# Kernel optimization log

Hardware: AMD Instinct MI355X
Metric: run time of the kernel (lower is better)

Reference implementation:

```python
import jax, jax.numpy as jnp
import numpy as np

NEG_BIG = -9e15
ALPHA = 0.2  # leakyrelu negative slope


def setup_inputs() -> dict:
    key = jax.random.key(0)
    k1, k2, k3, k4 = jax.random.split(key, 4)
    N, F_in, F_out = 8192, 256, 256
    h = jax.random.normal(k1, (N, F_in), dtype=jnp.float32)
    adj = jax.random.randint(k2, (N, N), 0, 2).astype(jnp.float32)
    W = jax.random.normal(k3, (F_in, F_out), dtype=jnp.float32) * (1.414 / np.sqrt(F_in))
    a = jax.random.normal(k4, (2 * F_out, 1), dtype=jnp.float32) * (1.414 / np.sqrt(2 * F_out))
    return {"h": h, "adj": adj, "W": W, "a": a}


def reference(h, adj, W, a):
    F_out = W.shape[1]
    Wh = h @ W  # [N, F_out]
    # Decomposed additive score: e_ij = leakyrelu(a1.Wh_i + a2.Wh_j)
    # identical to matmul(cat([Wh_i, Wh_j]), a) in the original.
    a1 = a[:F_out, 0]  # [F_out]
    a2 = a[F_out:, 0]  # [F_out]
    s1 = Wh @ a1  # [N]
    s2 = Wh @ a2  # [N]
    e = jax.nn.leaky_relu(s1[:, None] + s2[None, :], negative_slope=ALPHA)  # [N, N]
    e = jnp.where(adj > 0, e, NEG_BIG)
    attention = jax.nn.softmax(e, axis=1)
    # dropout skipped (eval mode: training=False)
    h_prime = attention @ Wh  # [N, F_out]
    return jax.nn.elu(h_prime)
```

## Files before the change

kernel.cpp:

```cpp
#include <hip/hip_runtime.h>
#include <hip/hip_bf16.h>

#define N 8192
#define F 256
#define KSPLIT 4
#define JBLK (N / KSPLIT)
#define NITER (JBLK / 64)
#define LOG2E 1.4426950408889634f

using s16x8 = __attribute__((ext_vector_type(8))) short;
using f32x4 = __attribute__((ext_vector_type(4))) float;

static __device__ __forceinline__ unsigned short f2bf(float f) {
  unsigned int u = __float_as_uint(f);
  unsigned int r = u + 0x7fffu + ((u >> 16) & 1u);
  return (unsigned short)(r >> 16);
}
static __device__ __forceinline__ float bf2f(unsigned short u) {
  return __uint_as_float(((unsigned int)u) << 16);
}
static __device__ __forceinline__ void glds16(const void* g, void* l) {
  __builtin_amdgcn_global_load_lds(
      (const __attribute__((address_space(1))) unsigned int*)g,
      (__attribute__((address_space(3))) unsigned int*)l, 16, 0, 0);
}

__global__ __launch_bounds__(256) void k0_wt(const float* __restrict__ W,
                                             unsigned short* __restrict__ Wt) {
  int k = blockIdx.x;
  int f = threadIdx.x;
  Wt[f * 256 + k] = f2bf(W[k * 256 + f]);
}

__global__ __launch_bounds__(256) void k1_wh(const float* __restrict__ h,
                                             const unsigned short* __restrict__ Wt,
                                             const float* __restrict__ a,
                                             char* __restrict__ WhbT,
                                             float* __restrict__ s1g,
                                             float* __restrict__ s2g) {
  __shared__ char lds[8192 + 32768];
  char* Alds = lds;
  char* Blds = lds + 8192;
  int t = threadIdx.x;
  int i0 = blockIdx.x * 64;
  int l = t & 63, w = t >> 6;
  int lr = l & 15, lk = l >> 4;
  f32x4 acc[4][4] = {};
  for (int kt = 0; kt < 4; ++kt) {
    int k0 = kt * 64;
    if (kt) __syncthreads();
#pragma unroll
    for (int c = 0; c < 4; ++c) {
      int flat = c * 256 + t;
      int i = flat >> 4, jc = flat & 15;
      float4 v = *reinterpret_cast<const float4*>(h + (size_t)(i0 + i) * 256 + k0 + jc * 4);
      ushort4 pk;
      pk.x = f2bf(v.x); pk.y = f2bf(v.y); pk.z = f2bf(v.z); pk.w = f2bf(v.w);
      *reinterpret_cast<ushort4*>(Alds + i * 128 + ((jc * 8) ^ ((i & 7) << 4))) = pk;
    }
#pragma unroll
    for (int c = 0; c < 8; ++c) {
      int idx = c * 256 + t;
      int fr = idx >> 3, kc = idx & 7;
      uint4 v = *reinterpret_cast<const uint4*>(Wt + fr * 256 + k0 + kc * 8);
      *reinterpret_cast<uint4*>(Blds + fr * 128 + ((kc * 16) ^ ((fr & 7) << 4))) = v;
    }
    __syncthreads();
#pragma unroll
    for (int kk = 0; kk < 2; ++kk) {
      int kofs = kk * 64 + lk * 16;
      s16x8 afr[4], bfr[4];
#pragma unroll
      for (int mf = 0; mf < 4; ++mf) {
        int ar = mf * 16 + lr;
        afr[mf] = *reinterpret_cast<const s16x8*>(Alds + ar * 128 + (kofs ^ ((ar & 7) << 4)));
      }
#pragma unroll
      for (int nf = 0; nf < 4; ++nf) {
        int br = w * 64 + nf * 16 + lr;
        bfr[nf] = *reinterpret_cast<const s16x8*>(Blds + br * 128 + (kofs ^ ((br & 7) << 4)));
      }
#pragma unroll
      for (int mf = 0; mf < 4; ++mf)
#pragma unroll
        for (int nf = 0; nf < 4; ++nf)
          acc[mf][nf] = __builtin_amdgcn_mfma_f32_16x16x32_bf16(afr[mf], bfr[nf], acc[mf][nf], 0, 0, 0);
    }
  }
  int tj = blockIdx.x;
#pragma unroll
  for (int mf = 0; mf < 4; ++mf) {
#pragma unroll
    for (int nf = 0; nf < 4; ++nf) {
      int f = w * 64 + nf * 16 + lr;
      int jj = mf * 16 + lk * 4;
      int kc = jj >> 3, sub = (jj >> 2) & 1;
      ushort4 pk;
      pk.x = f2bf(acc[mf][nf][0]);
      pk.y = f2bf(acc[mf][nf][1]);
      pk.z = f2bf(acc[mf][nf][2]);
      pk.w = f2bf(acc[mf][nf][3]);
      *reinterpret_cast<ushort4*>(WhbT + (size_t)tj * 32768 + f * 128 +
                                  ((kc * 16) ^ ((f & 7) << 4)) + sub * 8) = pk;
    }
  }
  float a1v[4], a2v[4];
#pragma unroll
  for (int nf = 0; nf < 4; ++nf) {
    int f = w * 64 + nf * 16 + lr;
    a1v[nf] = a[f];
    a2v[nf] = a[256 + f];
  }
  float* s1l = (float*)lds;
  float* s2l = s1l + 64;
  __syncthreads();
  if (t < 128) s1l[t] = 0.f;
  __syncthreads();
#pragma unroll
  for (int mf = 0; mf < 4; ++mf) {
#pragma unroll
    for (int r = 0; r < 4; ++r) {
      float p1 = 0.f, p2 = 0.f;
#pragma unroll
      for (int nf = 0; nf < 4; ++nf) {
        p1 += acc[mf][nf][r] * a1v[nf];
        p2 += acc[mf][nf][r] * a2v[nf];
      }
      p1 += __shfl_xor(p1, 1); p1 += __shfl_xor(p1, 2);
      p1 += __shfl_xor(p1, 4); p1 += __shfl_xor(p1, 8);
      p2 += __shfl_xor(p2, 1); p2 += __shfl_xor(p2, 2);
      p2 += __shfl_xor(p2, 4); p2 += __shfl_xor(p2, 8);
      if (lr == 0) {
        atomicAdd(&s1l[mf * 16 + lk * 4 + r], p1);
        atomicAdd(&s2l[mf * 16 + lk * 4 + r], p2);
      }
    }
  }
  __syncthreads();
  if (t < 64) {
    s1g[i0 + t] = s1l[t] * LOG2E;
    s2g[i0 + t] = s2l[t] * LOG2E;
  }
}

__global__ __launch_bounds__(512) void k3_attn(const float* __restrict__ adj,
                                               const char* __restrict__ WhbT,
                                               const float* __restrict__ s1,
                                               const float* __restrict__ s2,
                                               float* __restrict__ numw,
                                               float* __restrict__ denw) {
  __shared__ char lds[2 * 32768 + 2 * 32768 + 8192];
  char* Abase = lds;
  char* Bbase = lds + 65536;
  float* s2l = (float*)(lds + 131072);
  int t = threadIdx.x, w = t >> 6, l = t & 63, lr = l & 15, lk = l >> 4;
  int i0 = blockIdx.x * 128;
  int ks = blockIdx.y;
  int jb = ks * JBLK;
  int r = w * 16 + lr;
  int row = i0 + r;
  float s1v = s1[row];

  *reinterpret_cast<float4*>(&s2l[t * 4]) = *reinterpret_cast<const float4*>(s2 + jb + t * 4);

  f32x4 acc[16] = {};
  float ds = 0.f;

#define STAGE(tile, buf)                                                        \
  {                                                                             \
    const char* gB = WhbT + (size_t)(ks * NITER + (tile)) * 32768 + w * 4096;   \
    char* lB = Bbase + (buf) * 32768 + w * 4096;                                \
    _Pragma("unroll") for (int c = 0; c < 4; ++c)                               \
        glds16(gB + c * 1024 + l * 16, lB + c * 1024);                          \
    char* lA = Abase + (buf) * 32768 + w * 4096;                                \
    _Pragma("unroll") for (int c = 0; c < 4; ++c) {                             \
      int rloc = w * 16 + c * 4 + (l >> 4);                                     \
      const float* srcA = adj + (size_t)(i0 + rloc) * N + jb + (tile) * 64 +    \
                          (((l & 15) ^ (rloc & 7)) << 2);                       \
      glds16(srcA, lA + c * 1024);                                              \
    }                                                                           \
  }

  STAGE(0, 0);
  __syncthreads();

  for (int it = 0; it < NITER; ++it) {
    int cb = it & 1;
    bool pf = (it + 1) < NITER;
    if (pf) {
      STAGE(it + 1, cb ^ 1);
      asm volatile("s_waitcnt vmcnt(8)" ::: "memory");
    } else {
      asm volatile("s_waitcnt vmcnt(0)" ::: "memory");
    }
    __builtin_amdgcn_s_barrier();

    const char* At = Abase + cb * 32768 + r * 256;
    s16x8 afr[2];
#pragma unroll
    for (int kk = 0; kk < 2; ++kk) {
      int G0 = kk * 8 + lk * 2;
      f32x4 av0 = *reinterpret_cast<const f32x4*>(At + ((G0 ^ (r & 7)) << 4));
      f32x4 av1 = *reinterpret_cast<const f32x4*>(At + (((G0 + 1) ^ (r & 7)) << 4));
      const float* sp = &s2l[it * 64 + kk * 32 + lk * 8];
      float4 sv0 = *reinterpret_cast<const float4*>(sp);
      float4 sv1 = *reinterpret_cast<const float4*>(sp + 4);
      s16x8 af;
#define PEL(e, av, sv)                                                          \
      {                                                                         \
        float x = s1v + (sv); x = fmaxf(x, 0.2f * x);                           \
        float p = (av) > 0.f ? exp2f(x) : 0.f;                                  \
        unsigned short us = (unsigned short)((__float_as_uint(p) + 0x8000u) >> 16); \
        ds += bf2f(us); af[e] = (short)us;                                      \
      }
      PEL(0, av0[0], sv0.x) PEL(1, av0[1], sv0.y) PEL(2, av0[2], sv0.z) PEL(3, av0[3], sv0.w)
      PEL(4, av1[0], sv1.x) PEL(5, av1[1], sv1.y) PEL(6, av1[2], sv1.z) PEL(7, av1[3], sv1.w)
#undef PEL
      afr[kk] = af;
    }
    const char* Bt = Bbase + cb * 32768;
#pragma unroll
    for (int kk = 0; kk < 2; ++kk) {
      int kofs = kk * 64 + lk * 16;
#pragma unroll
      for (int nf = 0; nf < 16; ++nf) {
        int br = nf * 16 + lr;
        s16x8 bfr = *reinterpret_cast<const s16x8*>(Bt + br * 128 + (kofs ^ ((br & 7) << 4)));
        acc[nf] = __builtin_amdgcn_mfma_f32_16x16x32_bf16(afr[kk], bfr, acc[nf], 0, 0, 0);
      }
    }
    asm volatile("s_waitcnt lgkmcnt(0)" ::: "memory");
    __builtin_amdgcn_s_barrier();
  }
#undef STAGE

  ds += __shfl_xor(ds, 16);
  ds += __shfl_xor(ds, 32);
  if (l < 16) denw[(size_t)ks * N + row] = ds;

  float* nump = numw + (size_t)ks * N * F;
#pragma unroll
  for (int nf = 0; nf < 16; ++nf) {
#pragma unroll
    for (int rr = 0; rr < 4; ++rr) {
      nump[(size_t)(i0 + w * 16 + lk * 4 + rr) * F + nf * 16 + lr] = acc[nf][rr];
    }
  }
}

__global__ __launch_bounds__(256) void k4_fin(const float* __restrict__ numw,
                                              const float* __restrict__ denw,
                                              float* __restrict__ out) {
  int idx = (blockIdx.x * 256 + threadIdx.x) * 4;
  int i = idx >> 8;
  float4 sn = {0.f, 0.f, 0.f, 0.f};
  float sd = 0.f;
#pragma unroll
  for (int ksp = 0; ksp < KSPLIT; ++ksp) {
    float4 v = *reinterpret_cast<const float4*>(numw + (size_t)ksp * N * F + idx);
    sn.x += v.x; sn.y += v.y; sn.z += v.z; sn.w += v.w;
    sd += denw[(size_t)ksp * N + i];
  }
  float r = 1.f / sd;
  float4 o;
  float hp;
  hp = sn.x * r; o.x = hp > 0.f ? hp : (__expf(hp) - 1.f);
  hp = sn.y * r; o.y = hp > 0.f ? hp : (__expf(hp) - 1.f);
  hp = sn.z * r; o.z = hp > 0.f ? hp : (__expf(hp) - 1.f);
  hp = sn.w * r; o.w = hp > 0.f ? hp : (__expf(hp) - 1.f);
  *reinterpret_cast<float4*>(out + idx) = o;
}

extern "C" void kernel_launch(void* const* d_in, const int* in_sizes, int n_in,
                              void* d_out, int out_size, void* d_ws, size_t ws_size,
                              hipStream_t stream) {
  const float* h   = (const float*)d_in[0];
  const float* adj = (const float*)d_in[1];
  const float* W   = (const float*)d_in[2];
  const float* a   = (const float*)d_in[3];
  float* out = (float*)d_out;

  char* ws = (char*)d_ws;
  size_t o = 0;
  char* WhbT           = ws + o;                    o += (size_t)4 * 1024 * 1024;
  float* s1            = (float*)(ws + o);          o += 32768;
  float* s2            = (float*)(ws + o);          o += 32768;
  float* denw          = (float*)(ws + o);          o += (size_t)KSPLIT * N * 4;
  unsigned short* Wt   = (unsigned short*)(ws + o); o += 131072;
  float* numw          = (float*)(ws + o);          o += (size_t)KSPLIT * N * F * 4;

  hipLaunchKernelGGL(k0_wt, dim3(256), dim3(256), 0, stream, W, Wt);
  hipLaunchKernelGGL(k1_wh, dim3(N / 64), dim3(256), 0, stream, h, Wt, a, WhbT, s1, s2);
  hipLaunchKernelGGL(k3_attn, dim3(N / 128, KSPLIT), dim3(512), 0, stream,
                     adj, WhbT, s1, s2, numw, denw);
  hipLaunchKernelGGL(k4_fin, dim3(N * F / 1024), dim3(256), 0, stream, numw, denw, out);
}
```

Baseline: 131.5 us.

## Load adj directly to registers, double rows per wave, split keys eightfold

The attention kernel no longer stages adjacency tiles through LDS. Each lane loads its adj values straight into registers, double-buffered across two unrolled iterations. Each wave now covers 32 rows with two accumulator sets that share every B fragment read from LDS, so block rows go from 128 to 256 and KSPLIT goes from 4 to 8. LDS use drops so two blocks can fit per CU, and reuse of B tiles from LDS doubles. The costs are higher register pressure (32 accumulator vectors plus 16 float4 adj buffers) under a two-block occupancy hint, and twice as much partial-sum traffic for the final reduction kernel.

```diff
diff --git a/kernel.cpp b/kernel.cpp
--- a/kernel.cpp
+++ b/kernel.cpp
@@ -3,7 +3,7 @@
 
 #define N 8192
 #define F 256
-#define KSPLIT 4
+#define KSPLIT 8
 #define JBLK (N / KSPLIT)
 #define NITER (JBLK / 64)
 #define LOG2E 1.4426950408889634f
@@ -143,107 +143,133 @@
   }
 }
 
-__global__ __launch_bounds__(512) void k3_attn(const float* __restrict__ adj,
-                                               const char* __restrict__ WhbT,
-                                               const float* __restrict__ s1,
-                                               const float* __restrict__ s2,
-                                               float* __restrict__ numw,
-                                               float* __restrict__ denw) {
-  __shared__ char lds[2 * 32768 + 2 * 32768 + 8192];
-  char* Abase = lds;
-  char* Bbase = lds + 65536;
-  float* s2l = (float*)(lds + 131072);
+__global__ __launch_bounds__(512, 2) void k3_attn(const float* __restrict__ adj,
+                                                  const char* __restrict__ WhbT,
+                                                  const float* __restrict__ s1,
+                                                  const float* __restrict__ s2,
+                                                  float* __restrict__ numw,
+                                                  float* __restrict__ denw) {
+  __shared__ char lds[2 * 32768 + 4096];
+  char* Bbase = lds;
+  float* s2l = (float*)(lds + 65536);
   int t = threadIdx.x, w = t >> 6, l = t & 63, lr = l & 15, lk = l >> 4;
-  int i0 = blockIdx.x * 128;
+  int i0 = blockIdx.x * 256;
   int ks = blockIdx.y;
   int jb = ks * JBLK;
-  int r = w * 16 + lr;
-  int row = i0 + r;
-  float s1v = s1[row];
-
-  *reinterpret_cast<float4*>(&s2l[t * 4]) = *reinterpret_cast<const float4*>(s2 + jb + t * 4);
-
-  f32x4 acc[16] = {};
-  float ds = 0.f;
-
-#define STAGE(tile, buf)                                                        \
+  int rowA = i0 + w * 32 + lr;
+  int rowB = rowA + 16;
+  float s1vA = s1[rowA], s1vB = s1[rowB];
+  const float* aArow = adj + (size_t)rowA * N + jb + lk * 8;
+  const float* aBrow = adj + (size_t)rowB * N + jb + lk * 8;
+
+  *reinterpret_cast<float2*>(&s2l[t * 2]) = *reinterpret_cast<const float2*>(s2 + jb + t * 2);
+
+  f32x4 acc0[16] = {}, acc1[16] = {};
+  float dsA = 0.f, dsB = 0.f;
+
+#define STAGE_B(tile, buf)                                                      \
   {                                                                             \
     const char* gB = WhbT + (size_t)(ks * NITER + (tile)) * 32768 + w * 4096;   \
     char* lB = Bbase + (buf) * 32768 + w * 4096;                                \
     _Pragma("unroll") for (int c = 0; c < 4; ++c)                               \
         glds16(gB + c * 1024 + l * 16, lB + c * 1024);                          \
-    char* lA = Abase + (buf) * 32768 + w * 4096;                                \
-    _Pragma("unroll") for (int c = 0; c < 4; ++c) {                             \
-      int rloc = w * 16 + c * 4 + (l >> 4);                                     \
-      const float* srcA = adj + (size_t)(i0 + rloc) * N + jb + (tile) * 64 +    \
-                          (((l & 15) ^ (rloc & 7)) << 2);                       \
-      glds16(srcA, lA + c * 1024);                                              \
+  }
+#define LOAD_ADJ(dst, tile)                                                     \
+  {                                                                             \
+    const float* pa = aArow + (tile) * 64;                                      \
+    const float* pb = aBrow + (tile) * 64;                                      \
+    dst[0] = *reinterpret_cast<const float4*>(pa);                              \
+    dst[1] = *reinterpret_cast<const float4*>(pa + 4);                          \
+    dst[2] = *reinterpret_cast<const float4*>(pa + 32);                         \
+    dst[3] = *reinterpret_cast<const float4*>(pa + 36);                         \
+    dst[4] = *reinterpret_cast<const float4*>(pb);                              \
+    dst[5] = *reinterpret_cast<const float4*>(pb + 4);                          \
+    dst[6] = *reinterpret_cast<const float4*>(pb + 32);                         \
+    dst[7] = *reinterpret_cast<const float4*>(pb + 36);                         \
+  }
+#define PEL(dst, e, av, sv, dsx)                                                \
+  {                                                                             \
+    float x = (dst##_s1) + (sv); x = fmaxf(x, 0.2f * x);                        \
+    float p = (av) > 0.f ? exp2f(x) : 0.f;                                      \
+    unsigned short us = (unsigned short)((__float_as_uint(p) + 0x8000u) >> 16); \
+    dsx += bf2f(us); dst[e] = (short)us;                                        \
+  }
+#define PFRAG(dst, a0, a1, sv0, sv1, dsx)                                       \
+  PEL(dst, 0, a0.x, sv0.x, dsx) PEL(dst, 1, a0.y, sv0.y, dsx)                   \
+  PEL(dst, 2, a0.z, sv0.z, dsx) PEL(dst, 3, a0.w, sv0.w, dsx)                   \
+  PEL(dst, 4, a1.x, sv1.x, dsx) PEL(dst, 5, a1.y, sv1.y, dsx)                   \
+  PEL(dst, 6, a1.z, sv1.z, dsx) PEL(dst, 7, a1.w, sv1.w, dsx)
+
+#define BODY(IT, CUR, NXT)                                                      \
+  {                                                                             \
+    const int it = (IT);                                                        \
+    int cb = it & 1;                                                            \
+    if (it + 1 < NITER) {                                                       \
+      STAGE_B(it + 1, cb ^ 1);                                                  \
+      LOAD_ADJ(NXT, it + 1);                                                    \
+      asm volatile("s_waitcnt vmcnt(12)" ::: "memory");                         \
+    } else {                                                                    \
+      asm volatile("s_waitcnt vmcnt(0)" ::: "memory");                          \
     }                                                                           \
-  }
-
-  STAGE(0, 0);
+    __builtin_amdgcn_s_barrier();                                               \
+    const float* sp = &s2l[it * 64 + lk * 8];                                   \
+    float4 sv00 = *reinterpret_cast<const float4*>(sp);                         \
+    float4 sv01 = *reinterpret_cast<const float4*>(sp + 4);                     \
+    float4 sv10 = *reinterpret_cast<const float4*>(sp + 32);                    \
+    float4 sv11 = *reinterpret_cast<const float4*>(sp + 36);                    \
+    s16x8 afA0, afA1, afB0, afB1;                                               \
+    float afA0_s1 = s1vA, afA1_s1 = s1vA, afB0_s1 = s1vB, afB1_s1 = s1vB;       \
+    (void)afA0_s1; (void)afA1_s1; (void)afB0_s1; (void)afB1_s1;                 \
+    PFRAG(afA0, CUR[0], CUR[1], sv00, sv01, dsA)                                \
+    PFRAG(afA1, CUR[2], CUR[3], sv10, sv11, dsA)                                \
+    PFRAG(afB0, CUR[4], CUR[5], sv00, sv01, dsB)                                \
+    PFRAG(afB1, CUR[6], CUR[7], sv10, sv11, dsB)                                \
+    const char* Bt = Bbase + cb * 32768;                                        \
+    _Pragma("unroll") for (int kk = 0; kk < 2; ++kk) {                          \
+      int kofs = kk * 64 + lk * 16;                                             \
+      s16x8 aA = kk ? afA1 : afA0;                                              \
+      s16x8 aB = kk ? afB1 : afB0;                                              \
+      _Pragma("unroll") for (int nf = 0; nf < 16; ++nf) {                       \
+        int br = nf * 16 + lr;                                                  \
+        s16x8 bfr = *reinterpret_cast<const s16x8*>(                            \
+            Bt + br * 128 + (kofs ^ ((br & 7) << 4)));                          \
+        acc0[nf] = __builtin_amdgcn_mfma_f32_16x16x32_bf16(aA, bfr, acc0[nf], 0, 0, 0); \
+        acc1[nf] = __builtin_amdgcn_mfma_f32_16x16x32_bf16(aB, bfr, acc1[nf], 0, 0, 0); \
+      }                                                                         \
+    }                                                                           \
+    asm volatile("s_waitcnt lgkmcnt(0)" ::: "memory");                          \
+    __builtin_amdgcn_s_barrier();                                               \
+  }
+
+  float4 ajP[8], ajQ[8];
+  STAGE_B(0, 0);
+  LOAD_ADJ(ajP, 0);
   __syncthreads();
 
-  for (int it = 0; it < NITER; ++it) {
-    int cb = it & 1;
-    bool pf = (it + 1) < NITER;
-    if (pf) {
-      STAGE(it + 1, cb ^ 1);
-      asm volatile("s_waitcnt vmcnt(8)" ::: "memory");
-    } else {
-      asm volatile("s_waitcnt vmcnt(0)" ::: "memory");
-    }
-    __builtin_amdgcn_s_barrier();
-
-    const char* At = Abase + cb * 32768 + r * 256;
-    s16x8 afr[2];
-#pragma unroll
-    for (int kk = 0; kk < 2; ++kk) {
-      int G0 = kk * 8 + lk * 2;
-      f32x4 av0 = *reinterpret_cast<const f32x4*>(At + ((G0 ^ (r & 7)) << 4));
-      f32x4 av1 = *reinterpret_cast<const f32x4*>(At + (((G0 + 1) ^ (r & 7)) << 4));
-      const float* sp = &s2l[it * 64 + kk * 32 + lk * 8];
-      float4 sv0 = *reinterpret_cast<const float4*>(sp);
-      float4 sv1 = *reinterpret_cast<const float4*>(sp + 4);
-      s16x8 af;
-#define PEL(e, av, sv)                                                          \
-      {                                                                         \
-        float x = s1v + (sv); x = fmaxf(x, 0.2f * x);                           \
-        float p = (av) > 0.f ? exp2f(x) : 0.f;                                  \
-        unsigned short us = (unsigned short)((__float_as_uint(p) + 0x8000u) >> 16); \
-        ds += bf2f(us); af[e] = (short)us;                                      \
-      }
-      PEL(0, av0[0], sv0.x) PEL(1, av0[1], sv0.y) PEL(2, av0[2], sv0.z) PEL(3, av0[3], sv0.w)
-      PEL(4, av1[0], sv1.x) PEL(5, av1[1], sv1.y) PEL(6, av1[2], sv1.z) PEL(7, av1[3], sv1.w)
+  for (int it2 = 0; it2 < NITER / 2; ++it2) {
+    BODY(2 * it2, ajP, ajQ);
+    BODY(2 * it2 + 1, ajQ, ajP);
+  }
+#undef BODY
+#undef PFRAG
 #undef PEL
-      afr[kk] = af;
-    }
-    const char* Bt = Bbase + cb * 32768;
-#pragma unroll
-    for (int kk = 0; kk < 2; ++kk) {
-      int kofs = kk * 64 + lk * 16;
-#pragma unroll
-      for (int nf = 0; nf < 16; ++nf) {
-        int br = nf * 16 + lr;
-        s16x8 bfr = *reinterpret_cast<const s16x8*>(Bt + br * 128 + (kofs ^ ((br & 7) << 4)));
-        acc[nf] = __builtin_amdgcn_mfma_f32_16x16x32_bf16(afr[kk], bfr, acc[nf], 0, 0, 0);
-      }
-    }
-    asm volatile("s_waitcnt lgkmcnt(0)" ::: "memory");
-    __builtin_amdgcn_s_barrier();
-  }
-#undef STAGE
-
-  ds += __shfl_xor(ds, 16);
-  ds += __shfl_xor(ds, 32);
-  if (l < 16) denw[(size_t)ks * N + row] = ds;
-
+#undef LOAD_ADJ
+#undef STAGE_B
+
+  dsA += __shfl_xor(dsA, 16); dsA += __shfl_xor(dsA, 32);
+  dsB += __shfl_xor(dsB, 16); dsB += __shfl_xor(dsB, 32);
+  if (l < 16) {
+    denw[(size_t)ks * N + rowA] = dsA;
+    denw[(size_t)ks * N + rowB] = dsB;
+  }
   float* nump = numw + (size_t)ks * N * F;
 #pragma unroll
   for (int nf = 0; nf < 16; ++nf) {
 #pragma unroll
     for (int rr = 0; rr < 4; ++rr) {
-      nump[(size_t)(i0 + w * 16 + lk * 4 + rr) * F + nf * 16 + lr] = acc[nf][rr];
+      int irow = i0 + w * 32 + lk * 4 + rr;
+      nump[(size_t)irow * F + nf * 16 + lr] = acc0[nf][rr];
+      nump[(size_t)(irow + 16) * F + nf * 16 + lr] = acc1[nf][rr];
     }
   }
 }
@@ -291,7 +317,7 @@
 
   hipLaunchKernelGGL(k0_wt, dim3(256), dim3(256), 0, stream, W, Wt);
   hipLaunchKernelGGL(k1_wh, dim3(N / 64), dim3(256), 0, stream, h, Wt, a, WhbT, s1, s2);
-  hipLaunchKernelGGL(k3_attn, dim3(N / 128, KSPLIT), dim3(512), 0, stream,
+  hipLaunchKernelGGL(k3_attn, dim3(N / 256, KSPLIT), dim3(512), 0, stream,
                      adj, WhbT, s1, s2, numw, denw);
   hipLaunchKernelGGL(k4_fin, dim3(N * F / 1024), dim3(256), 0, stream, numw, denw, out);
 }
```

New measurement: 327.0 us. 2.49x slower.

## Double k-split to 8 and shrink attention tiles to 32 columns

Applied to the files above, without the earlier changes.

Raises the column split of the attention kernel from 4 to 8 so twice as many blocks run, and halves each pipeline tile to 32 columns, which halves LDS use per block. The projection kernel now writes the bf16 transposed Wh in a new 32-column tile layout with a matching swizzle, and the attention loop is rewritten to do one k-step per iteration. The aim is more occupancy and parallelism, paid for with twice as many partial numerator/denominator writes for the reduction and more barriers per column processed.

```diff
diff --git a/kernel.cpp b/kernel.cpp
--- a/kernel.cpp
+++ b/kernel.cpp
@@ -3,9 +3,9 @@
 
 #define N 8192
 #define F 256
-#define KSPLIT 4
+#define KSPLIT 8
 #define JBLK (N / KSPLIT)
-#define NITER (JBLK / 64)
+#define NITER (JBLK / 32)
 #define LOG2E 1.4426950408889634f
 
 using s16x8 = __attribute__((ext_vector_type(8))) short;
@@ -87,21 +87,22 @@
           acc[mf][nf] = __builtin_amdgcn_mfma_f32_16x16x32_bf16(afr[mf], bfr[nf], acc[mf][nf], 0, 0, 0);
     }
   }
-  int tj = blockIdx.x;
 #pragma unroll
   for (int mf = 0; mf < 4; ++mf) {
 #pragma unroll
     for (int nf = 0; nf < 4; ++nf) {
       int f = w * 64 + nf * 16 + lr;
-      int jj = mf * 16 + lk * 4;
-      int kc = jj >> 3, sub = (jj >> 2) & 1;
+      int tj32 = blockIdx.x * 2 + (mf >> 1);
+      int g = ((mf & 1) << 1) + (lk >> 1);
+      int sub = lk & 1;
+      int fp = f >> 1;
+      int u = ((((f & 1) << 2) + g) ^ (fp & 7));
       ushort4 pk;
       pk.x = f2bf(acc[mf][nf][0]);
       pk.y = f2bf(acc[mf][nf][1]);
       pk.z = f2bf(acc[mf][nf][2]);
       pk.w = f2bf(acc[mf][nf][3]);
-      *reinterpret_cast<ushort4*>(WhbT + (size_t)tj * 32768 + f * 128 +
-                                  ((kc * 16) ^ ((f & 7) << 4)) + sub * 8) = pk;
+      *reinterpret_cast<ushort4*>(WhbT + (size_t)tj32 * 16384 + fp * 128 + u * 16 + sub * 8) = pk;
     }
   }
   float a1v[4], a2v[4];
@@ -149,34 +150,33 @@
                                                const float* __restrict__ s2,
                                                float* __restrict__ numw,
                                                float* __restrict__ denw) {
-  __shared__ char lds[2 * 32768 + 2 * 32768 + 8192];
+  __shared__ char lds[2 * 16384 + 2 * 16384 + 4096];
   char* Abase = lds;
-  char* Bbase = lds + 65536;
-  float* s2l = (float*)(lds + 131072);
+  char* Bbase = lds + 32768;
+  float* s2l = (float*)(lds + 65536);
   int t = threadIdx.x, w = t >> 6, l = t & 63, lr = l & 15, lk = l >> 4;
   int i0 = blockIdx.x * 128;
   int ks = blockIdx.y;
   int jb = ks * JBLK;
-  int r = w * 16 + lr;
-  int row = i0 + r;
+  int row = i0 + w * 16 + lr;
   float s1v = s1[row];
 
-  *reinterpret_cast<float4*>(&s2l[t * 4]) = *reinterpret_cast<const float4*>(s2 + jb + t * 4);
+  *reinterpret_cast<float2*>(&s2l[t * 2]) = *reinterpret_cast<const float2*>(s2 + jb + t * 2);
 
   f32x4 acc[16] = {};
   float ds = 0.f;
 
 #define STAGE(tile, buf)                                                        \
   {                                                                             \
-    const char* gB = WhbT + (size_t)(ks * NITER + (tile)) * 32768 + w * 4096;   \
-    char* lB = Bbase + (buf) * 32768 + w * 4096;                                \
-    _Pragma("unroll") for (int c = 0; c < 4; ++c)                               \
+    const char* gB = WhbT + (size_t)(ks * NITER + (tile)) * 16384 + w * 2048;   \
+    char* lB = Bbase + (buf) * 16384 + w * 2048;                                \
+    _Pragma("unroll") for (int c = 0; c < 2; ++c)                               \
         glds16(gB + c * 1024 + l * 16, lB + c * 1024);                          \
-    char* lA = Abase + (buf) * 32768 + w * 4096;                                \
-    _Pragma("unroll") for (int c = 0; c < 4; ++c) {                             \
-      int rloc = w * 16 + c * 4 + (l >> 4);                                     \
-      const float* srcA = adj + (size_t)(i0 + rloc) * N + jb + (tile) * 64 +    \
-                          (((l & 15) ^ (rloc & 7)) << 2);                       \
+    char* lA = Abase + (buf) * 16384 + w * 2048;                                \
+    _Pragma("unroll") for (int c = 0; c < 2; ++c) {                             \
+      int lr8 = c * 8 + (l >> 3);                                               \
+      const float* srcA = adj + (size_t)(i0 + w * 16 + lr8) * N + jb +          \
+                          (tile) * 32 + (((l & 7) ^ (lr8 & 7)) << 2);           \
       glds16(srcA, lA + c * 1024);                                              \
     }                                                                           \
   }
@@ -186,48 +186,40 @@
 
   for (int it = 0; it < NITER; ++it) {
     int cb = it & 1;
-    bool pf = (it + 1) < NITER;
-    if (pf) {
+    if (it + 1 < NITER) {
       STAGE(it + 1, cb ^ 1);
-      asm volatile("s_waitcnt vmcnt(8)" ::: "memory");
+      asm volatile("s_waitcnt vmcnt(4)" ::: "memory");
     } else {
       asm volatile("s_waitcnt vmcnt(0)" ::: "memory");
     }
     __builtin_amdgcn_s_barrier();
 
-    const char* At = Abase + cb * 32768 + r * 256;
-    s16x8 afr[2];
-#pragma unroll
-    for (int kk = 0; kk < 2; ++kk) {
-      int G0 = kk * 8 + lk * 2;
-      f32x4 av0 = *reinterpret_cast<const f32x4*>(At + ((G0 ^ (r & 7)) << 4));
-      f32x4 av1 = *reinterpret_cast<const f32x4*>(At + (((G0 + 1) ^ (r & 7)) << 4));
-      const float* sp = &s2l[it * 64 + kk * 32 + lk * 8];
-      float4 sv0 = *reinterpret_cast<const float4*>(sp);
-      float4 sv1 = *reinterpret_cast<const float4*>(sp + 4);
-      s16x8 af;
+    const char* At = Abase + cb * 16384 + w * 2048 + lr * 128;
+    f32x4 av0 = *reinterpret_cast<const f32x4*>(At + (((lk << 1) ^ (lr & 7)) << 4));
+    f32x4 av1 = *reinterpret_cast<const f32x4*>(At + ((((lk << 1) | 1) ^ (lr & 7)) << 4));
+    const float* sp = &s2l[it * 32 + lk * 8];
+    float4 sv0 = *reinterpret_cast<const float4*>(sp);
+    float4 sv1 = *reinterpret_cast<const float4*>(sp + 4);
+    s16x8 afr;
 #define PEL(e, av, sv)                                                          \
-      {                                                                         \
-        float x = s1v + (sv); x = fmaxf(x, 0.2f * x);                           \
-        float p = (av) > 0.f ? exp2f(x) : 0.f;                                  \
-        unsigned short us = (unsigned short)((__float_as_uint(p) + 0x8000u) >> 16); \
-        ds += bf2f(us); af[e] = (short)us;                                      \
-      }
-      PEL(0, av0[0], sv0.x) PEL(1, av0[1], sv0.y) PEL(2, av0[2], sv0.z) PEL(3, av0[3], sv0.w)
-      PEL(4, av1[0], sv1.x) PEL(5, av1[1], sv1.y) PEL(6, av1[2], sv1.z) PEL(7, av1[3], sv1.w)
+    {                                                                           \
+      float x = s1v + (sv); x = fmaxf(x, 0.2f * x);                             \
+      float p = (av) > 0.f ? exp2f(x) : 0.f;                                    \
+      unsigned short us = (unsigned short)((__float_as_uint(p) + 0x8000u) >> 16); \
+      ds += bf2f(us); afr[e] = (short)us;                                       \
+    }
+    PEL(0, av0[0], sv0.x) PEL(1, av0[1], sv0.y) PEL(2, av0[2], sv0.z) PEL(3, av0[3], sv0.w)
+    PEL(4, av1[0], sv1.x) PEL(5, av1[1], sv1.y) PEL(6, av1[2], sv1.z) PEL(7, av1[3], sv1.w)
 #undef PEL
-      afr[kk] = af;
-    }
-    const char* Bt = Bbase + cb * 32768;
-#pragma unroll
-    for (int kk = 0; kk < 2; ++kk) {
-      int kofs = kk * 64 + lk * 16;
-#pragma unroll
-      for (int nf = 0; nf < 16; ++nf) {
-        int br = nf * 16 + lr;
-        s16x8 bfr = *reinterpret_cast<const s16x8*>(Bt + br * 128 + (kofs ^ ((br & 7) << 4)));
-        acc[nf] = __builtin_amdgcn_mfma_f32_16x16x32_bf16(afr[kk], bfr, acc[nf], 0, 0, 0);
-      }
+
+    const char* Bt = Bbase + cb * 16384;
+#pragma unroll
+    for (int nf = 0; nf < 16; ++nf) {
+      int br = nf * 16 + lr;
+      int fp = br >> 1;
+      int u = ((((br & 1) << 2) + lk) ^ (fp & 7));
+      s16x8 bfr = *reinterpret_cast<const s16x8*>(Bt + fp * 128 + u * 16);
+      acc[nf] = __builtin_amdgcn_mfma_f32_16x16x32_bf16(afr, bfr, acc[nf], 0, 0, 0);
     }
     asm volatile("s_waitcnt lgkmcnt(0)" ::: "memory");
     __builtin_amdgcn_s_barrier();
```

Result: no change. 133.9 us (+1.8%).

## Fuse finalize into attention kernel and drop the column split-K

Applied to the files above, without the earlier changes.

Removes the 4-way column split and the separate finalize kernel. Each 512-thread block now handles 32 rows over all N columns, with its waves split into 2 row groups × 4 feature groups. It normalizes by the row sum and applies ELU directly to the output. This eliminates writing and re-reading the split-K partial numerators and denominators, plus one kernel launch. In exchange, every block streams the whole bf16 Wh matrix, so shared-Wh traffic rises about fourfold. The exp/score computation is also repeated by the four feature-group waves that share the same rows.

```diff
diff --git a/kernel.cpp b/kernel.cpp
--- a/kernel.cpp
+++ b/kernel.cpp
@@ -3,9 +3,7 @@
 
 #define N 8192
 #define F 256
-#define KSPLIT 4
-#define JBLK (N / KSPLIT)
-#define NITER (JBLK / 64)
+#define NITER (N / 64)
 #define LOG2E 1.4426950408889634f
 
 using s16x8 = __attribute__((ext_vector_type(8))) short;
@@ -147,61 +145,60 @@
                                                const char* __restrict__ WhbT,
                                                const float* __restrict__ s1,
                                                const float* __restrict__ s2,
-                                               float* __restrict__ numw,
-                                               float* __restrict__ denw) {
-  __shared__ char lds[2 * 32768 + 2 * 32768 + 8192];
-  char* Abase = lds;
-  char* Bbase = lds + 65536;
-  float* s2l = (float*)(lds + 131072);
+                                               float* __restrict__ out) {
+  __shared__ char lds[2 * 32768 + 2 * 8192 + 32768 + 256];
+  char* Bbase = lds;
+  char* Abase = lds + 65536;
+  float* s2l = (float*)(lds + 81920);
+  float* denl = (float*)(lds + 114688);
   int t = threadIdx.x, w = t >> 6, l = t & 63, lr = l & 15, lk = l >> 4;
-  int i0 = blockIdx.x * 128;
-  int ks = blockIdx.y;
-  int jb = ks * JBLK;
-  int r = w * 16 + lr;
-  int row = i0 + r;
+  int rg = w & 1, fg = w >> 1;
+  int i0 = blockIdx.x * 32;
+  int row = i0 + rg * 16 + lr;
   float s1v = s1[row];
 
-  *reinterpret_cast<float4*>(&s2l[t * 4]) = *reinterpret_cast<const float4*>(s2 + jb + t * 4);
-
-  f32x4 acc[16] = {};
+#pragma unroll
+  for (int c = 0; c < 4; ++c) {
+    *reinterpret_cast<float4*>(&s2l[t * 16 + c * 4]) =
+        *reinterpret_cast<const float4*>(s2 + t * 16 + c * 4);
+  }
+
+  f32x4 acc[4] = {};
   float ds = 0.f;
 
 #define STAGE(tile, buf)                                                        \
   {                                                                             \
-    const char* gB = WhbT + (size_t)(ks * NITER + (tile)) * 32768 + w * 4096;   \
+    const char* gB = WhbT + (size_t)(tile) * 32768 + w * 4096;                  \
     char* lB = Bbase + (buf) * 32768 + w * 4096;                                \
     _Pragma("unroll") for (int c = 0; c < 4; ++c)                               \
         glds16(gB + c * 1024 + l * 16, lB + c * 1024);                          \
-    char* lA = Abase + (buf) * 32768 + w * 4096;                                \
-    _Pragma("unroll") for (int c = 0; c < 4; ++c) {                             \
-      int rloc = w * 16 + c * 4 + (l >> 4);                                     \
-      const float* srcA = adj + (size_t)(i0 + rloc) * N + jb + (tile) * 64 +    \
-                          (((l & 15) ^ (rloc & 7)) << 2);                       \
-      glds16(srcA, lA + c * 1024);                                              \
-    }                                                                           \
+    int arow_l = w * 4 + (l >> 4);                                              \
+    const float* srcA = adj + (size_t)(i0 + arow_l) * N + (tile) * 64 +         \
+                        (((l & 15) ^ (arow_l & 7)) << 2);                       \
+    glds16(srcA, Abase + (buf) * 8192 + w * 1024);                              \
   }
 
   STAGE(0, 0);
   __syncthreads();
 
   for (int it = 0; it < NITER; ++it) {
-    int cb = it & 1;
-    bool pf = (it + 1) < NITER;
-    if (pf) {
-      STAGE(it + 1, cb ^ 1);
-      asm volatile("s_waitcnt vmcnt(8)" ::: "memory");
+    int buf = it & 1;
+    if (it + 1 < NITER) {
+      STAGE(it + 1, buf ^ 1);
+      asm volatile("s_waitcnt vmcnt(5)" ::: "memory");
     } else {
       asm volatile("s_waitcnt vmcnt(0)" ::: "memory");
     }
     __builtin_amdgcn_s_barrier();
 
-    const char* At = Abase + cb * 32768 + r * 256;
+    const char* At = Abase + buf * 8192 + (rg * 16 + lr) * 256;
+    int rs = lr & 7;
     s16x8 afr[2];
 #pragma unroll
     for (int kk = 0; kk < 2; ++kk) {
-      int G0 = kk * 8 + lk * 2;
-      f32x4 av0 = *reinterpret_cast<const f32x4*>(At + ((G0 ^ (r & 7)) << 4));
-      f32x4 av1 = *reinterpret_cast<const f32x4*>(At + (((G0 + 1) ^ (r & 7)) << 4));
+      int g0 = kk * 8 + lk * 2;
+      f32x4 av0 = *reinterpret_cast<const f32x4*>(At + ((g0 ^ rs) << 4));
+      f32x4 av1 = *reinterpret_cast<const f32x4*>(At + (((g0 + 1) ^ rs) << 4));
       const float* sp = &s2l[it * 64 + kk * 32 + lk * 8];
       float4 sv0 = *reinterpret_cast<const float4*>(sp);
       float4 sv1 = *reinterpret_cast<const float4*>(sp + 4);
@@ -218,13 +215,13 @@
 #undef PEL
       afr[kk] = af;
     }
-    const char* Bt = Bbase + cb * 32768;
+    const char* Bt = Bbase + buf * 32768;
 #pragma unroll
     for (int kk = 0; kk < 2; ++kk) {
       int kofs = kk * 64 + lk * 16;
 #pragma unroll
-      for (int nf = 0; nf < 16; ++nf) {
-        int br = nf * 16 + lr;
+      for (int nf = 0; nf < 4; ++nf) {
+        int br = fg * 64 + nf * 16 + lr;
         s16x8 bfr = *reinterpret_cast<const s16x8*>(Bt + br * 128 + (kofs ^ ((br & 7) << 4)));
         acc[nf] = __builtin_amdgcn_mfma_f32_16x16x32_bf16(afr[kk], bfr, acc[nf], 0, 0, 0);
       }
@@ -236,39 +233,21 @@
 
   ds += __shfl_xor(ds, 16);
   ds += __shfl_xor(ds, 32);
-  if (l < 16) denw[(size_t)ks * N + row] = ds;
-
-  float* nump = numw + (size_t)ks * N * F;
-#pragma unroll
-  for (int nf = 0; nf < 16; ++nf) {
+  if (fg == 0 && lk == 0) denl[rg * 16 + lr] = ds;
+  __syncthreads();
+
+  float rd[4];
+#pragma unroll
+  for (int rr = 0; rr < 4; ++rr) rd[rr] = 1.f / denl[rg * 16 + lk * 4 + rr];
+#pragma unroll
+  for (int nf = 0; nf < 4; ++nf) {
 #pragma unroll
     for (int rr = 0; rr < 4; ++rr) {
-      nump[(size_t)(i0 + w * 16 + lk * 4 + rr) * F + nf * 16 + lr] = acc[nf][rr];
-    }
-  }
-}
-
-__global__ __launch_bounds__(256) void k4_fin(const float* __restrict__ numw,
-                                              const float* __restrict__ denw,
-                                              float* __restrict__ out) {
-  int idx = (blockIdx.x * 256 + threadIdx.x) * 4;
-  int i = idx >> 8;
-  float4 sn = {0.f, 0.f, 0.f, 0.f};
-  float sd = 0.f;
-#pragma unroll
-  for (int ksp = 0; ksp < KSPLIT; ++ksp) {
-    float4 v = *reinterpret_cast<const float4*>(numw + (size_t)ksp * N * F + idx);
-    sn.x += v.x; sn.y += v.y; sn.z += v.z; sn.w += v.w;
-    sd += denw[(size_t)ksp * N + i];
-  }
-  float r = 1.f / sd;
-  float4 o;
-  float hp;
-  hp = sn.x * r; o.x = hp > 0.f ? hp : (__expf(hp) - 1.f);
-  hp = sn.y * r; o.y = hp > 0.f ? hp : (__expf(hp) - 1.f);
-  hp = sn.z * r; o.z = hp > 0.f ? hp : (__expf(hp) - 1.f);
-  hp = sn.w * r; o.w = hp > 0.f ? hp : (__expf(hp) - 1.f);
-  *reinterpret_cast<float4*>(out + idx) = o;
+      float hp = acc[nf][rr] * rd[rr];
+      float o = hp > 0.f ? hp : (__expf(hp) - 1.f);
+      out[(size_t)(i0 + rg * 16 + lk * 4 + rr) * F + fg * 64 + nf * 16 + lr] = o;
+    }
+  }
 }
 
 extern "C" void kernel_launch(void* const* d_in, const int* in_sizes, int n_in,
@@ -285,13 +264,10 @@
   char* WhbT           = ws + o;                    o += (size_t)4 * 1024 * 1024;
   float* s1            = (float*)(ws + o);          o += 32768;
   float* s2            = (float*)(ws + o);          o += 32768;
-  float* denw          = (float*)(ws + o);          o += (size_t)KSPLIT * N * 4;
   unsigned short* Wt   = (unsigned short*)(ws + o); o += 131072;
-  float* numw          = (float*)(ws + o);          o += (size_t)KSPLIT * N * F * 4;
 
   hipLaunchKernelGGL(k0_wt, dim3(256), dim3(256), 0, stream, W, Wt);
   hipLaunchKernelGGL(k1_wh, dim3(N / 64), dim3(256), 0, stream, h, Wt, a, WhbT, s1, s2);
-  hipLaunchKernelGGL(k3_attn, dim3(N / 128, KSPLIT), dim3(512), 0, stream,
-                     adj, WhbT, s1, s2, numw, denw);
-  hipLaunchKernelGGL(k4_fin, dim3(N * F / 1024), dim3(256), 0, stream, numw, denw, out);
-}
+  hipLaunchKernelGGL(k3_attn, dim3(N / 32), dim3(512), 0, stream,
+                     adj, WhbT, s1, s2, out);
+}
```

Result: slower. 249.6 us (+89.8%).
